# Kernel optimization log

Measured on AMD Instinct MI355X. Metric: run time of the kernel, lower is better.

The kernel has to match this reference:

```python
import jax, jax.numpy as jnp
import numpy as np

N_EMBD = 2048
H_I = 16   # indexer heads
D_I = 32   # indexer dim


def setup_inputs() -> dict:
    key = jax.random.key(0)
    k1, k2, k3, k4 = jax.random.split(key, 4)
    x = jax.random.normal(k1, (2, 4096, N_EMBD), dtype=jnp.float32)
    # nn.Linear(in, out, bias=False) weights, stored (out, in) like torch
    s = 1.0 / np.sqrt(N_EMBD)
    Wq = jax.random.uniform(k2, (H_I * D_I, N_EMBD), jnp.float32, -s, s)
    Wk = jax.random.uniform(k3, (D_I, N_EMBD), jnp.float32, -s, s)
    Ww = jax.random.uniform(k4, (H_I, N_EMBD), jnp.float32, -s, s)
    return {"x": x, "Wq": Wq, "Wk": Wk, "Ww": Ww}


def reference(x, Wq, Wk, Ww):
    B, T, C = x.shape
    q = (x @ Wq.T).reshape(B, T, H_I, D_I)   # (B,T,H,D)
    k = x @ Wk.T                              # (B,T,D)
    w = x @ Ww.T                              # (B,T,H)
    scores = jnp.einsum('bqhd,bkd->bqhk', q, k)
    scores = jax.nn.relu(scores)
    importance = jnp.einsum('bqh,bqhk->bqk', w, scores)  # (B,T,T)
    return importance
```

## Files before the change

kernel.cpp:

```cpp
#include <hip/hip_runtime.h>
#include <hip/hip_bf16.h>
#include <stdint.h>


typedef __attribute__((ext_vector_type(8))) short bf16x8;
typedef __attribute__((ext_vector_type(4))) float f32x4;
typedef __attribute__((ext_vector_type(2))) __fp16 f16x2;

__device__ __forceinline__ unsigned short f2bf(float f) {
  union { float f; unsigned u; } c; c.f = f;
  unsigned u = c.u;
  u += 0x7FFFu + ((u >> 16) & 1u);
  return (unsigned short)(u >> 16);
}

__device__ __forceinline__ f16x2 u32_to_h2(unsigned u) {
  union { unsigned u; f16x2 h; } c; c.u = u; return c.h;
}
__device__ __forceinline__ unsigned h2_to_u32(f16x2 h) {
  union { unsigned u; f16x2 h; } c; c.h = h; return c.u;
}

__device__ __forceinline__ void async_copy16(void* lds, const void* g) {
  __builtin_amdgcn_global_load_lds(
      (const __attribute__((address_space(1))) unsigned*)g,
      (__attribute__((address_space(3))) unsigned*)lds, 16, 0, 0);
}

__global__ __launch_bounds__(256) void pack_kernel(
    const float* __restrict__ x, const float* __restrict__ Wq,
    const float* __restrict__ Wk, const float* __restrict__ Ww,
    unsigned short* __restrict__ xb, unsigned short* __restrict__ Wp) {
  const int64_t NX4 = 16777216 / 4;
  int64_t i = (int64_t)blockIdx.x * 256 + threadIdx.x;
  if (i < NX4) {
    float4 v = ((const float4*)x)[i];
    ushort4 o;
    o.x = f2bf(v.x); o.y = f2bf(v.y); o.z = f2bf(v.z); o.w = f2bf(v.w);
    ((ushort4*)xb)[i] = o;
  } else {
    int p = (int)(i - NX4);
    int row = p >> 9;
    int col = (p & 511) << 2;
    float4 v = make_float4(0.f, 0.f, 0.f, 0.f);
    if (row < 512)      v = *(const float4*)(Wq + (int64_t)row * 2048 + col);
    else if (row < 544) v = *(const float4*)(Wk + (int64_t)(row - 512) * 2048 + col);
    else if (row < 560) v = *(const float4*)(Ww + (int64_t)(row - 544) * 2048 + col);
    ushort4 o;
    o.x = f2bf(v.x); o.y = f2bf(v.y); o.z = f2bf(v.z); o.w = f2bf(v.w);
    ((ushort4*)Wp)[p] = o;
  }
}

__global__ __launch_bounds__(256) void gemm_proj(
    const unsigned short* __restrict__ xb, const unsigned short* __restrict__ Wp,
    unsigned short* __restrict__ qh, unsigned short* __restrict__ kh,
    float* __restrict__ wf) {
  __shared__ short lds_a[64 * 32];
  __shared__ short lds_b[128 * 32];
  const int tid = threadIdx.x;
  const int lane = tid & 63;
  const int l15 = lane & 15, quad = lane >> 4;
  const int wave = tid >> 6;
  const int wn = wave;
  const int m0 = blockIdx.y * 64, n0 = blockIdx.x * 128;

  const int c0 = tid, c1 = tid + 256;
  const unsigned short* ga  = xb + (int64_t)(m0 + (tid >> 2)) * 2048 + (tid & 3) * 8;
  const unsigned short* gb0 = Wp + (int64_t)(n0 + (c0 >> 2)) * 2048 + (c0 & 3) * 8;
  const unsigned short* gb1 = Wp + (int64_t)(n0 + (c1 >> 2)) * 2048 + (c1 & 3) * 8;

  f32x4 acc[4][2] = {};

  for (int kt = 0; kt < 64; ++kt) {
    const int ko = kt * 32;
    async_copy16(&lds_a[tid * 8], ga + ko);
    async_copy16(&lds_b[c0 * 8], gb0 + ko);
    async_copy16(&lds_b[c1 * 8], gb1 + ko);
    __syncthreads();
    bf16x8 af[4], bfr[2];
#pragma unroll
    for (int i = 0; i < 4; ++i)
      af[i] = *(const bf16x8*)&lds_a[(i * 16 + l15) * 32 + quad * 8];
#pragma unroll
    for (int j = 0; j < 2; ++j)
      bfr[j] = *(const bf16x8*)&lds_b[(wn * 32 + j * 16 + l15) * 32 + quad * 8];
#pragma unroll
    for (int i = 0; i < 4; ++i)
#pragma unroll
      for (int j = 0; j < 2; ++j)
        acc[i][j] = __builtin_amdgcn_mfma_f32_16x16x32_bf16(af[i], bfr[j], acc[i][j], 0, 0, 0);
    __syncthreads();
  }

#pragma unroll
  for (int i = 0; i < 4; ++i)
#pragma unroll
    for (int j = 0; j < 2; ++j)
#pragma unroll
      for (int r = 0; r < 4; ++r) {
        int m = m0 + i * 16 + quad * 4 + r;
        int n = n0 + wn * 32 + j * 16 + l15;
        float v = acc[i][j][r];
        if (n < 512)      qh[((int64_t)(n >> 5) * 8192 + m) * 32 + (n & 31)] = f2bf(v);
        else if (n < 544) kh[(int64_t)m * 32 + (n - 512)] = f2bf(v);
        else if (n < 560) wf[m * 16 + (n - 544)] = v;
      }
}

__global__ __launch_bounds__(256) void scores_kernel(
    const unsigned short* __restrict__ qh, const unsigned short* __restrict__ kh,
    const float* __restrict__ wf, float* __restrict__ out) {
  const int kt = blockIdx.x, qt = blockIdx.y, b = blockIdx.z;
  const int tid = threadIdx.x;
  const int lane = tid & 63;
  const int l15 = lane & 15, quad = lane >> 4;
  const int wave = tid >> 6;
  const int wk = wave & 1, wq = wave >> 1;

  __shared__ unsigned w2[8][132];

  const int qrow0 = b * 4096 + qt * 128;
  const int krow0 = b * 4096 + kt * 128;

  {
    const float4* ws = (const float4*)(wf + (int64_t)qrow0 * 16);
#pragma unroll
    for (int r = 0; r < 2; ++r) {
      int f = tid * 2 + r;
      float4 v = ws[f];
      int row = f >> 2, hb = (f & 3) * 4;
      f16x2 p01, p23;
      p01.x = (__fp16)v.x; p01.y = (__fp16)v.y;
      p23.x = (__fp16)v.z; p23.y = (__fp16)v.w;
      w2[(hb >> 1) + 0][row] = h2_to_u32(p01);
      w2[(hb >> 1) + 1][row] = h2_to_u32(p23);
    }
  }

  bf16x8 ka[4];
#pragma unroll
  for (int i = 0; i < 4; ++i) {
    int kk = krow0 + wk * 64 + i * 16 + l15;
    ka[i] = *(const bf16x8*)&kh[(int64_t)kk * 32 + quad * 8];
  }

  const unsigned short* qbase =
      qh + (int64_t)(qrow0 + wq * 64 + l15) * 32 + quad * 8;

  f32x4 acc[4][4] = {};
  __syncthreads();

  const f16x2 hz = u32_to_h2(0u);
  const f32x4 z = {0.f, 0.f, 0.f, 0.f};

#pragma unroll
  for (int hp = 0; hp < 8; ++hp) {
    bf16x8 q0[4], q1[4];
#pragma unroll
    for (int j = 0; j < 4; ++j) {
      q0[j] = *(const bf16x8*)&qbase[(int64_t)(2 * hp) * 262144 + j * 512];
      q1[j] = *(const bf16x8*)&qbase[(int64_t)(2 * hp + 1) * 262144 + j * 512];
    }
    f16x2 wv[4];
#pragma unroll
    for (int j = 0; j < 4; ++j)
      wv[j] = u32_to_h2(w2[hp][wq * 64 + j * 16 + l15]);

#pragma unroll
    for (int i = 0; i < 4; ++i)
#pragma unroll
      for (int j = 0; j < 4; ++j) {
        f32x4 t0 = __builtin_amdgcn_mfma_f32_16x16x32_bf16(ka[i], q0[j], z, 0, 0, 0);
        f32x4 t1 = __builtin_amdgcn_mfma_f32_16x16x32_bf16(ka[i], q1[j], z, 0, 0, 0);
#pragma unroll
        for (int r = 0; r < 4; ++r) {
          f16x2 p = __builtin_amdgcn_cvt_pkrtz(t0[r], t1[r]);
          p = __builtin_elementwise_max(p, hz);
          acc[i][j][r] = __builtin_amdgcn_fdot2(p, wv[j], acc[i][j][r], false);
        }
      }
  }

#pragma unroll
  for (int i = 0; i < 4; ++i)
#pragma unroll
    for (int j = 0; j < 4; ++j) {
      int q = qt * 128 + wq * 64 + j * 16 + l15;
      int k = kt * 128 + wk * 64 + i * 16 + quad * 4;
      float4 v = make_float4(acc[i][j][0], acc[i][j][1], acc[i][j][2], acc[i][j][3]);
      *(float4*)&out[((int64_t)b * 4096 + q) * 4096 + k] = v;
    }
}

extern "C" void kernel_launch(void* const* d_in, const int* in_sizes, int n_in,
                              void* d_out, int out_size, void* d_ws, size_t ws_size,
                              hipStream_t stream) {
  const float* x  = (const float*)d_in[0];
  const float* Wq = (const float*)d_in[1];
  const float* Wk = (const float*)d_in[2];
  const float* Ww = (const float*)d_in[3];
  float* out = (float*)d_out;

  char* ws = (char*)d_ws;
  unsigned short* xb = (unsigned short*)ws;
  unsigned short* Wp = (unsigned short*)(ws + 33554432);
  unsigned short* qh = (unsigned short*)(ws + 36175872);
  unsigned short* kh = (unsigned short*)(ws + 44564480);
  float*          wf = (float*)(ws + 45088768);

  pack_kernel<<<17664, 256, 0, stream>>>(x, Wq, Wk, Ww, xb, Wp);
  gemm_proj<<<dim3(5, 128), 256, 0, stream>>>(xb, Wp, qh, kh, wf);
  scores_kernel<<<dim3(32, 32, 2), 256, 0, stream>>>(qh, kh, wf, out);
}
```

Baseline: 284.9 us.

## Double-buffer projection GEMM LDS tiles and widen K step to 64

The projection GEMM now uses two LDS buffers per operand and a K tile of 64 instead of 32. The next tile's async global-to-LDS copies are issued before the MFMAs on the current tile, so each iteration needs one barrier instead of two. This is meant to hide global load latency and halve loop and barrier overhead, at the cost of four times the LDS per block and a 128-byte row stride that may cause more LDS bank conflicts.

Measured after the change: 291.7 us. +2.4%, slower.

```diff
diff --git a/kernel.cpp b/kernel.cpp
--- a/kernel.cpp
+++ b/kernel.cpp
@@ -56,8 +56,8 @@
     const unsigned short* __restrict__ xb, const unsigned short* __restrict__ Wp,
     unsigned short* __restrict__ qh, unsigned short* __restrict__ kh,
     float* __restrict__ wf) {
-  __shared__ short lds_a[64 * 32];
-  __shared__ short lds_b[128 * 32];
+  __shared__ short lds_a[2][64 * 64];
+  __shared__ short lds_b[2][128 * 64];
   const int tid = threadIdx.x;
   const int lane = tid & 63;
   const int l15 = lane & 15, quad = lane >> 4;
@@ -65,33 +65,57 @@
   const int wn = wave;
   const int m0 = blockIdx.y * 64, n0 = blockIdx.x * 128;
 
-  const int c0 = tid, c1 = tid + 256;
-  const unsigned short* ga  = xb + (int64_t)(m0 + (tid >> 2)) * 2048 + (tid & 3) * 8;
-  const unsigned short* gb0 = Wp + (int64_t)(n0 + (c0 >> 2)) * 2048 + (c0 & 3) * 8;
-  const unsigned short* gb1 = Wp + (int64_t)(n0 + (c1 >> 2)) * 2048 + (c1 & 3) * 8;
-
   f32x4 acc[4][2] = {};
 
-  for (int kt = 0; kt < 64; ++kt) {
-    const int ko = kt * 32;
-    async_copy16(&lds_a[tid * 8], ga + ko);
-    async_copy16(&lds_b[c0 * 8], gb0 + ko);
-    async_copy16(&lds_b[c1 * 8], gb1 + ko);
+#define STAGE_A(buf, ko)                                                        \
+  {                                                                             \
+    _Pragma("unroll") for (int cc = 0; cc < 2; ++cc) {                          \
+      int c = tid + cc * 256;                                                   \
+      async_copy16(&lds_a[buf][c * 8],                                          \
+                   xb + (int64_t)(m0 + (c >> 3)) * 2048 + (ko) + (c & 7) * 8);  \
+    }                                                                           \
+  }
+#define STAGE_B(buf, ko)                                                        \
+  {                                                                             \
+    _Pragma("unroll") for (int cc = 0; cc < 4; ++cc) {                          \
+      int c = tid + cc * 256;                                                   \
+      async_copy16(&lds_b[buf][c * 8],                                          \
+                   Wp + (int64_t)(n0 + (c >> 3)) * 2048 + (ko) + (c & 7) * 8);  \
+    }                                                                           \
+  }
+
+  STAGE_A(0, 0);
+  STAGE_B(0, 0);
+  __syncthreads();
+
+  for (int kt = 0; kt < 32; ++kt) {
+    const int cur = kt & 1, nxt = cur ^ 1;
+    if (kt < 31) {
+      STAGE_A(nxt, (kt + 1) * 64);
+      STAGE_B(nxt, (kt + 1) * 64);
+    }
+    bf16x8 af[4][2], bfr[2][2];
+#pragma unroll
+    for (int i = 0; i < 4; ++i)
+#pragma unroll
+      for (int s = 0; s < 2; ++s)
+        af[i][s] = *(const bf16x8*)&lds_a[cur][(i * 16 + l15) * 64 + s * 32 + quad * 8];
+#pragma unroll
+    for (int j = 0; j < 2; ++j)
+#pragma unroll
+      for (int s = 0; s < 2; ++s)
+        bfr[j][s] = *(const bf16x8*)&lds_b[cur][(wn * 32 + j * 16 + l15) * 64 + s * 32 + quad * 8];
+#pragma unroll
+    for (int s = 0; s < 2; ++s)
+#pragma unroll
+      for (int i = 0; i < 4; ++i)
+#pragma unroll
+        for (int j = 0; j < 2; ++j)
+          acc[i][j] = __builtin_amdgcn_mfma_f32_16x16x32_bf16(af[i][s], bfr[j][s], acc[i][j], 0, 0, 0);
     __syncthreads();
-    bf16x8 af[4], bfr[2];
-#pragma unroll
-    for (int i = 0; i < 4; ++i)
-      af[i] = *(const bf16x8*)&lds_a[(i * 16 + l15) * 32 + quad * 8];
-#pragma unroll
-    for (int j = 0; j < 2; ++j)
-      bfr[j] = *(const bf16x8*)&lds_b[(wn * 32 + j * 16 + l15) * 32 + quad * 8];
-#pragma unroll
-    for (int i = 0; i < 4; ++i)
-#pragma unroll
-      for (int j = 0; j < 2; ++j)
-        acc[i][j] = __builtin_amdgcn_mfma_f32_16x16x32_bf16(af[i], bfr[j], acc[i][j], 0, 0, 0);
-    __syncthreads();
-  }
+  }
+#undef STAGE_A
+#undef STAGE_B
 
 #pragma unroll
   for (int i = 0; i < 4; ++i)
```
